# Kernel optimization log

Measured on AMD Instinct MI355X. Metric: run time of the kernel, lower is better.

The kernel has to match this reference:

```python
import jax, jax.numpy as jnp
import numpy as np

N_NODES = 50000
N_EDGES = 625000
D_IN = 128
D_OUT = 128


def setup_inputs() -> dict:
    key = jax.random.key(0)
    k1, k2, k3 = jax.random.split(key, 3)
    x = jax.random.normal(k1, (N_NODES, D_IN), dtype=jnp.float32)
    edge_index = jax.random.randint(k2, (2, N_EDGES), 0, N_NODES, dtype=jnp.int64)
    # torch Linear weight: [d_out, d_in], Kaiming-uniform-ish scale
    weight = jax.random.normal(k3, (D_OUT, D_IN), dtype=jnp.float32) * (1.0 / np.sqrt(D_IN))
    bias = jnp.zeros((D_OUT,), dtype=jnp.float32)
    return {"x": x, "edge_index": edge_index, "weight": weight, "bias": bias}


def reference(x, edge_index, weight, bias):
    N = x.shape[0]
    # gcn_norm: add self-loops with weight 1.0 (improved=False)
    loop = jnp.arange(N, dtype=edge_index.dtype)
    src = jnp.concatenate([edge_index[0], loop])  # [E+N] message sources (x_j)
    dst = jnp.concatenate([edge_index[1], loop])  # [E+N] aggregation targets
    ew = jnp.ones(src.shape[0], dtype=x.dtype)
    # degree computed on target index (col), symmetric normalization
    deg = jax.ops.segment_sum(ew, dst, num_segments=N)
    dinv = jnp.where(deg > 0, jax.lax.rsqrt(deg), 0.0).astype(x.dtype)
    norm = dinv[src] * ew * dinv[dst]  # [E+N]
    # message: norm_e * x[src]; aggregate: scatter-add at dst
    agg = jax.ops.segment_sum(norm[:, None] * x[src], dst, num_segments=N)  # [N, d_in]
    # Linear
    return agg @ weight.T + bias
```

## Files before the change

kernel.cpp:

```cpp
#include <hip/hip_runtime.h>
#include <hip/hip_bf16.h>

#define N_NODES 50000
#define N_EDGES 625000
#define D 128
#define CAP 64
#define NTILES ((N_NODES + 15) / 16)
#define GRID_XW 1024
#define NRANGE 8
#define RSPAN (N_NODES / NRANGE)
#define PART_BLOCKS 1024
#define PART_STRIDE ((PART_BLOCKS / NRANGE) * 256)

typedef __attribute__((ext_vector_type(8))) short bf16x8;
typedef __attribute__((ext_vector_type(4))) float f32x4;

__device__ __forceinline__ float b2f(short s) {
    unsigned u = ((unsigned)(unsigned short)s) << 16;
    return __uint_as_float(u);
}
__device__ __forceinline__ short f2b(float f) {
    union { __hip_bfloat16 h; short s; } cv;
    cv.h = __float2bfloat16(f);
    return cv.s;
}

__global__ void k_zero(int* __restrict__ deg) {
    int i = blockIdx.x * 256 + threadIdx.x;
    if (i < N_NODES) deg[i] = 0;
}

__global__ __launch_bounds__(256) void k_fillpad(const int* __restrict__ src,
                                                 const int* __restrict__ dst,
                                                 int* __restrict__ deg,
                                                 int* __restrict__ colp) {
    int g = blockIdx.x & 7;
    int bg = blockIdx.x >> 3;
    int lo = g * RSPAN, hi = lo + RSPAN;
    for (int e = bg * 256 + threadIdx.x; e < N_EDGES; e += PART_STRIDE) {
        int d = dst[e];
        if (d >= lo && d < hi) {
            int p = atomicAdd(&deg[d], 1);
            if (p < CAP) colp[d * CAP + p] = src[e];
        }
    }
}

__global__ __launch_bounds__(256) void k_xw(const float* __restrict__ x,
                                            const float* __restrict__ w,
                                            const int* __restrict__ deg,
                                            short* __restrict__ y) {
    int t = threadIdx.x;
    int wave = t >> 6, lane = t & 63;
    int c0 = wave * 32;
    int lr = lane & 15;
    int lk = (lane >> 4) * 8;

    bf16x8 wf0[4], wf1[4];
    {
        const float* wp0 = w + (size_t)(c0 + lr) * D + lk;
        const float* wp1 = wp0 + 16 * D;
        #pragma unroll
        for (int ks = 0; ks < 4; ++ks) {
            f32x4 wa0 = *(const f32x4*)(wp0 + ks * 32);
            f32x4 wb0 = *(const f32x4*)(wp0 + ks * 32 + 4);
            f32x4 wa1 = *(const f32x4*)(wp1 + ks * 32);
            f32x4 wb1 = *(const f32x4*)(wp1 + ks * 32 + 4);
            #pragma unroll
            for (int q = 0; q < 4; ++q) {
                wf0[ks][q] = f2b(wa0[q]); wf0[ks][q + 4] = f2b(wb0[q]);
                wf1[ks][q] = f2b(wa1[q]); wf1[ks][q + 4] = f2b(wb1[q]);
            }
        }
    }

    for (int tile = blockIdx.x; tile < NTILES; tile += GRID_XW) {
        int row0 = tile * 16;
        const float* ap = x + (size_t)(row0 + lr) * D + lk;
        f32x4 acc0 = {0.f, 0.f, 0.f, 0.f};
        f32x4 acc1 = {0.f, 0.f, 0.f, 0.f};
        #pragma unroll
        for (int ks = 0; ks < 4; ++ks) {
            f32x4 xa = *(const f32x4*)(ap + ks * 32);
            f32x4 xb = *(const f32x4*)(ap + ks * 32 + 4);
            bf16x8 a;
            #pragma unroll
            for (int q = 0; q < 4; ++q) { a[q] = f2b(xa[q]); a[q + 4] = f2b(xb[q]); }
            acc0 = __builtin_amdgcn_mfma_f32_16x16x32_bf16(a, wf0[ks], acc0, 0, 0, 0);
            acc1 = __builtin_amdgcn_mfma_f32_16x16x32_bf16(a, wf1[ks], acc1, 0, 0, 0);
        }
        int orow = row0 + (lane >> 4) * 4;
        int oc0 = c0 + lr, oc1 = c0 + 16 + lr;
        #pragma unroll
        for (int i = 0; i < 4; ++i) {
            int r = orow + i;
            float ds = rsqrtf((float)(deg[r] + 1));
            y[(size_t)r * D + oc0] = f2b(acc0[i] * ds);
            y[(size_t)r * D + oc1] = f2b(acc1[i] * ds);
        }
    }
}

__global__ __launch_bounds__(256) void k_gather(const short* __restrict__ y,
                                                const int* __restrict__ deg,
                                                const int* __restrict__ colp,
                                                const float* __restrict__ bias,
                                                float* __restrict__ out) {
    int tid = blockIdx.x * 256 + threadIdx.x;
    int n = tid >> 4;
    int sub = threadIdx.x & 15;
    if (n >= N_NODES) return;
    int dn = deg[n];
    float dd = rsqrtf((float)(dn + 1));
    if (dn > CAP) dn = CAP;
    bf16x8 self = *(const bf16x8*)(y + (size_t)n * D + sub * 8);
    float acc0[8], acc1[8];
    #pragma unroll
    for (int q = 0; q < 8; ++q) { acc0[q] = b2f(self[q]); acc1[q] = 0.f; }
    const int* cp = colp + (size_t)n * CAP;
    int j = 0;
    for (; j + 4 <= dn; j += 4) {
        int s0 = cp[j + 0];
        int s1 = cp[j + 1];
        int s2 = cp[j + 2];
        int s3 = cp[j + 3];
        bf16x8 v0 = *(const bf16x8*)(y + (size_t)s0 * D + sub * 8);
        bf16x8 v1 = *(const bf16x8*)(y + (size_t)s1 * D + sub * 8);
        bf16x8 v2 = *(const bf16x8*)(y + (size_t)s2 * D + sub * 8);
        bf16x8 v3 = *(const bf16x8*)(y + (size_t)s3 * D + sub * 8);
        #pragma unroll
        for (int q = 0; q < 8; ++q) {
            acc0[q] += b2f(v0[q]) + b2f(v2[q]);
            acc1[q] += b2f(v1[q]) + b2f(v3[q]);
        }
    }
    for (; j < dn; ++j) {
        int s0 = cp[j];
        bf16x8 v0 = *(const bf16x8*)(y + (size_t)s0 * D + sub * 8);
        #pragma unroll
        for (int q = 0; q < 8; ++q) acc0[q] += b2f(v0[q]);
    }
    const float4* bch = (const float4*)(bias + sub * 8);
    float4 bb0 = bch[0], bb1 = bch[1];
    float4 o0, o1;
    o0.x = dd * (acc0[0] + acc1[0]) + bb0.x; o0.y = dd * (acc0[1] + acc1[1]) + bb0.y;
    o0.z = dd * (acc0[2] + acc1[2]) + bb0.z; o0.w = dd * (acc0[3] + acc1[3]) + bb0.w;
    o1.x = dd * (acc0[4] + acc1[4]) + bb1.x; o1.y = dd * (acc0[5] + acc1[5]) + bb1.y;
    o1.z = dd * (acc0[6] + acc1[6]) + bb1.z; o1.w = dd * (acc0[7] + acc1[7]) + bb1.w;
    float4* op = (float4*)(out + (size_t)n * D + sub * 8);
    op[0] = o0; op[1] = o1;
}

extern "C" void kernel_launch(void* const* d_in, const int* in_sizes, int n_in,
                              void* d_out, int out_size, void* d_ws, size_t ws_size,
                              hipStream_t stream) {
    const float* x    = (const float*)d_in[0];
    const int*   ei   = (const int*)d_in[1];
    const float* w    = (const float*)d_in[2];
    const float* bias = (const float*)d_in[3];
    float* out = (float*)d_out;

    const int* src = ei;
    const int* dst = ei + N_EDGES;

    char* p = (char*)d_ws;
    short* y  = (short*)p;  p += (size_t)N_NODES * D * 2;
    int* deg  = (int*)p;    p += (size_t)N_NODES * 4;
    int* colp = (int*)p;    p += (size_t)N_NODES * CAP * 4;

    k_zero<<<(N_NODES + 255) / 256, 256, 0, stream>>>(deg);
    k_fillpad<<<PART_BLOCKS, 256, 0, stream>>>(src, dst, deg, colp);
    k_xw<<<GRID_XW, 256, 0, stream>>>(x, w, deg, y);
    k_gather<<<((N_NODES * 16) + 255) / 256, 256, 0, stream>>>(y, deg, colp, bias, out);
}
```

Measured before the change: 91.47 us.

## Prefetch next x tile in xw kernel and shuffle-broadcast neighbor indices in gather

In the XW GEMM kernel, the next tile's x rows are loaded into registers before the current tile's MFMAs run, a software-pipelined prefetch meant to hide global load latency. In the gather kernel, each 16-lane group loads up to 16 neighbor indices cooperatively, one per lane, and broadcasts them with __shfl. The unroll is raised to 8 outstanding row loads. This cuts redundant per-lane index loads and adds memory-level parallelism, at the cost of more registers and shuffle instructions.

```diff
diff --git a/kernel.cpp b/kernel.cpp
--- a/kernel.cpp
+++ b/kernel.cpp
@@ -74,22 +74,47 @@
         }
     }
 
-    for (int tile = blockIdx.x; tile < NTILES; tile += GRID_XW) {
-        int row0 = tile * 16;
-        const float* ap = x + (size_t)(row0 + lr) * D + lk;
+    int tile = blockIdx.x;
+    f32x4 xcur0, xcur1, xcur2, xcur3, xcur4, xcur5, xcur6, xcur7;
+    {
+        const float* ap = x + (size_t)(tile * 16 + lr) * D + lk;
+        xcur0 = *(const f32x4*)(ap + 0);   xcur1 = *(const f32x4*)(ap + 4);
+        xcur2 = *(const f32x4*)(ap + 32);  xcur3 = *(const f32x4*)(ap + 36);
+        xcur4 = *(const f32x4*)(ap + 64);  xcur5 = *(const f32x4*)(ap + 68);
+        xcur6 = *(const f32x4*)(ap + 96);  xcur7 = *(const f32x4*)(ap + 100);
+    }
+    for (;;) {
+        int next = tile + GRID_XW;
+        bool has = next < NTILES;
+        f32x4 xn0, xn1, xn2, xn3, xn4, xn5, xn6, xn7;
+        if (has) {
+            const float* ap = x + (size_t)(next * 16 + lr) * D + lk;
+            xn0 = *(const f32x4*)(ap + 0);   xn1 = *(const f32x4*)(ap + 4);
+            xn2 = *(const f32x4*)(ap + 32);  xn3 = *(const f32x4*)(ap + 36);
+            xn4 = *(const f32x4*)(ap + 64);  xn5 = *(const f32x4*)(ap + 68);
+            xn6 = *(const f32x4*)(ap + 96);  xn7 = *(const f32x4*)(ap + 100);
+        }
         f32x4 acc0 = {0.f, 0.f, 0.f, 0.f};
         f32x4 acc1 = {0.f, 0.f, 0.f, 0.f};
-        #pragma unroll
-        for (int ks = 0; ks < 4; ++ks) {
-            f32x4 xa = *(const f32x4*)(ap + ks * 32);
-            f32x4 xb = *(const f32x4*)(ap + ks * 32 + 4);
-            bf16x8 a;
-            #pragma unroll
-            for (int q = 0; q < 4; ++q) { a[q] = f2b(xa[q]); a[q + 4] = f2b(xb[q]); }
-            acc0 = __builtin_amdgcn_mfma_f32_16x16x32_bf16(a, wf0[ks], acc0, 0, 0, 0);
-            acc1 = __builtin_amdgcn_mfma_f32_16x16x32_bf16(a, wf1[ks], acc1, 0, 0, 0);
-        }
-        int orow = row0 + (lane >> 4) * 4;
+        bf16x8 a;
+        #pragma unroll
+        for (int q = 0; q < 4; ++q) { a[q] = f2b(xcur0[q]); a[q + 4] = f2b(xcur1[q]); }
+        acc0 = __builtin_amdgcn_mfma_f32_16x16x32_bf16(a, wf0[0], acc0, 0, 0, 0);
+        acc1 = __builtin_amdgcn_mfma_f32_16x16x32_bf16(a, wf1[0], acc1, 0, 0, 0);
+        #pragma unroll
+        for (int q = 0; q < 4; ++q) { a[q] = f2b(xcur2[q]); a[q + 4] = f2b(xcur3[q]); }
+        acc0 = __builtin_amdgcn_mfma_f32_16x16x32_bf16(a, wf0[1], acc0, 0, 0, 0);
+        acc1 = __builtin_amdgcn_mfma_f32_16x16x32_bf16(a, wf1[1], acc1, 0, 0, 0);
+        #pragma unroll
+        for (int q = 0; q < 4; ++q) { a[q] = f2b(xcur4[q]); a[q + 4] = f2b(xcur5[q]); }
+        acc0 = __builtin_amdgcn_mfma_f32_16x16x32_bf16(a, wf0[2], acc0, 0, 0, 0);
+        acc1 = __builtin_amdgcn_mfma_f32_16x16x32_bf16(a, wf1[2], acc1, 0, 0, 0);
+        #pragma unroll
+        for (int q = 0; q < 4; ++q) { a[q] = f2b(xcur6[q]); a[q + 4] = f2b(xcur7[q]); }
+        acc0 = __builtin_amdgcn_mfma_f32_16x16x32_bf16(a, wf0[3], acc0, 0, 0, 0);
+        acc1 = __builtin_amdgcn_mfma_f32_16x16x32_bf16(a, wf1[3], acc1, 0, 0, 0);
+
+        int orow = tile * 16 + (lane >> 4) * 4;
         int oc0 = c0 + lr, oc1 = c0 + 16 + lr;
         #pragma unroll
         for (int i = 0; i < 4; ++i) {
@@ -98,6 +123,10 @@
             y[(size_t)r * D + oc0] = f2b(acc0[i] * ds);
             y[(size_t)r * D + oc1] = f2b(acc1[i] * ds);
         }
+        if (!has) break;
+        tile = next;
+        xcur0 = xn0; xcur1 = xn1; xcur2 = xn2; xcur3 = xn3;
+        xcur4 = xn4; xcur5 = xn5; xcur6 = xn6; xcur7 = xn7;
     }
 }
 
@@ -109,37 +138,70 @@
     int tid = blockIdx.x * 256 + threadIdx.x;
     int n = tid >> 4;
     int sub = threadIdx.x & 15;
+    int lane = threadIdx.x & 63;
+    int gb = lane & 48;
     if (n >= N_NODES) return;
-    int dn = deg[n];
-    float dd = rsqrtf((float)(dn + 1));
-    if (dn > CAP) dn = CAP;
+    int dn_raw = deg[n];
+    float dd = rsqrtf((float)(dn_raw + 1));
+    int dn = dn_raw < CAP ? dn_raw : CAP;
     bf16x8 self = *(const bf16x8*)(y + (size_t)n * D + sub * 8);
     float acc0[8], acc1[8];
     #pragma unroll
     for (int q = 0; q < 8; ++q) { acc0[q] = b2f(self[q]); acc1[q] = 0.f; }
     const int* cp = colp + (size_t)n * CAP;
-    int j = 0;
-    for (; j + 4 <= dn; j += 4) {
-        int s0 = cp[j + 0];
-        int s1 = cp[j + 1];
-        int s2 = cp[j + 2];
-        int s3 = cp[j + 3];
-        bf16x8 v0 = *(const bf16x8*)(y + (size_t)s0 * D + sub * 8);
-        bf16x8 v1 = *(const bf16x8*)(y + (size_t)s1 * D + sub * 8);
-        bf16x8 v2 = *(const bf16x8*)(y + (size_t)s2 * D + sub * 8);
-        bf16x8 v3 = *(const bf16x8*)(y + (size_t)s3 * D + sub * 8);
-        #pragma unroll
-        for (int q = 0; q < 8; ++q) {
-            acc0[q] += b2f(v0[q]) + b2f(v2[q]);
-            acc1[q] += b2f(v1[q]) + b2f(v3[q]);
-        }
-    }
-    for (; j < dn; ++j) {
-        int s0 = cp[j];
-        bf16x8 v0 = *(const bf16x8*)(y + (size_t)s0 * D + sub * 8);
-        #pragma unroll
-        for (int q = 0; q < 8; ++q) acc0[q] += b2f(v0[q]);
-    }
+
+    for (int bj = 0; bj < dn; bj += 16) {
+        int rem = dn - bj;
+        int m = rem < 16 ? rem : 16;
+        int cidx = (sub < m) ? cp[bj + sub] : 0;
+        int j = 0;
+        for (; j + 8 <= m; j += 8) {
+            int s0 = __shfl(cidx, gb + j + 0);
+            int s1 = __shfl(cidx, gb + j + 1);
+            int s2 = __shfl(cidx, gb + j + 2);
+            int s3 = __shfl(cidx, gb + j + 3);
+            int s4 = __shfl(cidx, gb + j + 4);
+            int s5 = __shfl(cidx, gb + j + 5);
+            int s6 = __shfl(cidx, gb + j + 6);
+            int s7 = __shfl(cidx, gb + j + 7);
+            bf16x8 v0 = *(const bf16x8*)(y + (size_t)s0 * D + sub * 8);
+            bf16x8 v1 = *(const bf16x8*)(y + (size_t)s1 * D + sub * 8);
+            bf16x8 v2 = *(const bf16x8*)(y + (size_t)s2 * D + sub * 8);
+            bf16x8 v3 = *(const bf16x8*)(y + (size_t)s3 * D + sub * 8);
+            bf16x8 v4 = *(const bf16x8*)(y + (size_t)s4 * D + sub * 8);
+            bf16x8 v5 = *(const bf16x8*)(y + (size_t)s5 * D + sub * 8);
+            bf16x8 v6 = *(const bf16x8*)(y + (size_t)s6 * D + sub * 8);
+            bf16x8 v7 = *(const bf16x8*)(y + (size_t)s7 * D + sub * 8);
+            #pragma unroll
+            for (int q = 0; q < 8; ++q) {
+                acc0[q] += b2f(v0[q]) + b2f(v2[q]) + b2f(v4[q]) + b2f(v6[q]);
+                acc1[q] += b2f(v1[q]) + b2f(v3[q]) + b2f(v5[q]) + b2f(v7[q]);
+            }
+        }
+        if (j + 4 <= m) {
+            int s0 = __shfl(cidx, gb + j + 0);
+            int s1 = __shfl(cidx, gb + j + 1);
+            int s2 = __shfl(cidx, gb + j + 2);
+            int s3 = __shfl(cidx, gb + j + 3);
+            bf16x8 v0 = *(const bf16x8*)(y + (size_t)s0 * D + sub * 8);
+            bf16x8 v1 = *(const bf16x8*)(y + (size_t)s1 * D + sub * 8);
+            bf16x8 v2 = *(const bf16x8*)(y + (size_t)s2 * D + sub * 8);
+            bf16x8 v3 = *(const bf16x8*)(y + (size_t)s3 * D + sub * 8);
+            #pragma unroll
+            for (int q = 0; q < 8; ++q) {
+                acc0[q] += b2f(v0[q]) + b2f(v2[q]);
+                acc1[q] += b2f(v1[q]) + b2f(v3[q]);
+            }
+            j += 4;
+        }
+        for (; j < m; ++j) {
+            int s0 = __shfl(cidx, gb + j);
+            bf16x8 v0 = *(const bf16x8*)(y + (size_t)s0 * D + sub * 8);
+            #pragma unroll
+            for (int q = 0; q < 8; ++q) acc0[q] += b2f(v0[q]);
+        }
+    }
+
     const float4* bch = (const float4*)(bias + sub * 8);
     float4 bb0 = bch[0], bb1 = bch[1];
     float4 o0, o1;
```

Measured after the change: 91.74 us. No clear change (+0.3%).

## Fuse fill and XW into one concurrent kernel, move source norm into gather

Applied to the files above, without the earlier changes.

Merges the CSR-pad fill and the X·W GEMM into a single launch whose blocks split by role, so the atomic-heavy fill overlaps the bandwidth-bound GEMM. Because y no longer has the finished degree available, the source-side normalization moves into the gather, which loads neighbor indices cooperatively and broadcasts index and rsqrt(deg) via shuffles. Neighbor indices are stored as 16-bit to halve colp traffic. The cost is extra deg lookups in the gather, and the 16-bit indices only fit because the node count is below 65536.

```diff
diff --git a/kernel.cpp b/kernel.cpp
--- a/kernel.cpp
+++ b/kernel.cpp
@@ -6,11 +6,11 @@
 #define D 128
 #define CAP 64
 #define NTILES ((N_NODES + 15) / 16)
-#define GRID_XW 1024
 #define NRANGE 8
 #define RSPAN (N_NODES / NRANGE)
-#define PART_BLOCKS 1024
-#define PART_STRIDE ((PART_BLOCKS / NRANGE) * 256)
+#define FILL_BLOCKS 1024
+#define XW_BLOCKS 1024
+#define PSTRIDE ((FILL_BLOCKS / NRANGE) * 256)
 
 typedef __attribute__((ext_vector_type(8))) short bf16x8;
 typedef __attribute__((ext_vector_type(4))) float f32x4;
@@ -30,116 +30,134 @@
     if (i < N_NODES) deg[i] = 0;
 }
 
-__global__ __launch_bounds__(256) void k_fillpad(const int* __restrict__ src,
-                                                 const int* __restrict__ dst,
-                                                 int* __restrict__ deg,
-                                                 int* __restrict__ colp) {
-    int g = blockIdx.x & 7;
-    int bg = blockIdx.x >> 3;
-    int lo = g * RSPAN, hi = lo + RSPAN;
-    for (int e = bg * 256 + threadIdx.x; e < N_EDGES; e += PART_STRIDE) {
-        int d = dst[e];
-        if (d >= lo && d < hi) {
-            int p = atomicAdd(&deg[d], 1);
-            if (p < CAP) colp[d * CAP + p] = src[e];
-        }
-    }
-}
-
-__global__ __launch_bounds__(256) void k_xw(const float* __restrict__ x,
-                                            const float* __restrict__ w,
-                                            const int* __restrict__ deg,
-                                            short* __restrict__ y) {
-    int t = threadIdx.x;
-    int wave = t >> 6, lane = t & 63;
-    int c0 = wave * 32;
-    int lr = lane & 15;
-    int lk = (lane >> 4) * 8;
-
-    bf16x8 wf0[4], wf1[4];
-    {
-        const float* wp0 = w + (size_t)(c0 + lr) * D + lk;
-        const float* wp1 = wp0 + 16 * D;
-        #pragma unroll
-        for (int ks = 0; ks < 4; ++ks) {
-            f32x4 wa0 = *(const f32x4*)(wp0 + ks * 32);
-            f32x4 wb0 = *(const f32x4*)(wp0 + ks * 32 + 4);
-            f32x4 wa1 = *(const f32x4*)(wp1 + ks * 32);
-            f32x4 wb1 = *(const f32x4*)(wp1 + ks * 32 + 4);
-            #pragma unroll
-            for (int q = 0; q < 4; ++q) {
-                wf0[ks][q] = f2b(wa0[q]); wf0[ks][q + 4] = f2b(wb0[q]);
-                wf1[ks][q] = f2b(wa1[q]); wf1[ks][q + 4] = f2b(wb1[q]);
+__global__ __launch_bounds__(256) void k_prep(const int* __restrict__ src,
+                                              const int* __restrict__ dst,
+                                              int* __restrict__ deg,
+                                              unsigned short* __restrict__ colp,
+                                              const float* __restrict__ x,
+                                              const float* __restrict__ w,
+                                              short* __restrict__ y) {
+    int b = blockIdx.x;
+    if (b < FILL_BLOCKS) {
+        int g = b & 7;
+        int bg = b >> 3;
+        int lo = g * RSPAN, hi = lo + RSPAN;
+        for (int e = bg * 256 + threadIdx.x; e < N_EDGES; e += PSTRIDE) {
+            int d = dst[e];
+            if (d >= lo && d < hi) {
+                int p = atomicAdd(&deg[d], 1);
+                if (p < CAP) colp[d * CAP + p] = (unsigned short)src[e];
             }
         }
-    }
+    } else {
+        int t = threadIdx.x;
+        int wave = t >> 6, lane = t & 63;
+        int c0 = wave * 32;
+        int lr = lane & 15;
+        int lk = (lane >> 4) * 8;
 
-    for (int tile = blockIdx.x; tile < NTILES; tile += GRID_XW) {
-        int row0 = tile * 16;
-        const float* ap = x + (size_t)(row0 + lr) * D + lk;
-        f32x4 acc0 = {0.f, 0.f, 0.f, 0.f};
-        f32x4 acc1 = {0.f, 0.f, 0.f, 0.f};
-        #pragma unroll
-        for (int ks = 0; ks < 4; ++ks) {
-            f32x4 xa = *(const f32x4*)(ap + ks * 32);
-            f32x4 xb = *(const f32x4*)(ap + ks * 32 + 4);
-            bf16x8 a;
+        bf16x8 wf0[4], wf1[4];
+        {
+            const float* wp0 = w + (size_t)(c0 + lr) * D + lk;
+            const float* wp1 = wp0 + 16 * D;
             #pragma unroll
-            for (int q = 0; q < 4; ++q) { a[q] = f2b(xa[q]); a[q + 4] = f2b(xb[q]); }
-            acc0 = __builtin_amdgcn_mfma_f32_16x16x32_bf16(a, wf0[ks], acc0, 0, 0, 0);
-            acc1 = __builtin_amdgcn_mfma_f32_16x16x32_bf16(a, wf1[ks], acc1, 0, 0, 0);
+            for (int ks = 0; ks < 4; ++ks) {
+                f32x4 wa0 = *(const f32x4*)(wp0 + ks * 32);
+                f32x4 wb0 = *(const f32x4*)(wp0 + ks * 32 + 4);
+                f32x4 wa1 = *(const f32x4*)(wp1 + ks * 32);
+                f32x4 wb1 = *(const f32x4*)(wp1 + ks * 32 + 4);
+                #pragma unroll
+                for (int q = 0; q < 4; ++q) {
+                    wf0[ks][q] = f2b(wa0[q]); wf0[ks][q + 4] = f2b(wb0[q]);
+                    wf1[ks][q] = f2b(wa1[q]); wf1[ks][q + 4] = f2b(wb1[q]);
+                }
+            }
         }
-        int orow = row0 + (lane >> 4) * 4;
-        int oc0 = c0 + lr, oc1 = c0 + 16 + lr;
-        #pragma unroll
-        for (int i = 0; i < 4; ++i) {
-            int r = orow + i;
-            float ds = rsqrtf((float)(deg[r] + 1));
-            y[(size_t)r * D + oc0] = f2b(acc0[i] * ds);
-            y[(size_t)r * D + oc1] = f2b(acc1[i] * ds);
+
+        for (int tile = b - FILL_BLOCKS; tile < NTILES; tile += XW_BLOCKS) {
+            int row0 = tile * 16;
+            const float* ap = x + (size_t)(row0 + lr) * D + lk;
+            f32x4 acc0 = {0.f, 0.f, 0.f, 0.f};
+            f32x4 acc1 = {0.f, 0.f, 0.f, 0.f};
+            #pragma unroll
+            for (int ks = 0; ks < 4; ++ks) {
+                f32x4 xa = *(const f32x4*)(ap + ks * 32);
+                f32x4 xb = *(const f32x4*)(ap + ks * 32 + 4);
+                bf16x8 a;
+                #pragma unroll
+                for (int q = 0; q < 4; ++q) { a[q] = f2b(xa[q]); a[q + 4] = f2b(xb[q]); }
+                acc0 = __builtin_amdgcn_mfma_f32_16x16x32_bf16(a, wf0[ks], acc0, 0, 0, 0);
+                acc1 = __builtin_amdgcn_mfma_f32_16x16x32_bf16(a, wf1[ks], acc1, 0, 0, 0);
+            }
+            int orow = row0 + (lane >> 4) * 4;
+            int oc0 = c0 + lr, oc1 = c0 + 16 + lr;
+            #pragma unroll
+            for (int i = 0; i < 4; ++i) {
+                y[(size_t)(orow + i) * D + oc0] = f2b(acc0[i]);
+                y[(size_t)(orow + i) * D + oc1] = f2b(acc1[i]);
+            }
         }
     }
 }
 
 __global__ __launch_bounds__(256) void k_gather(const short* __restrict__ y,
                                                 const int* __restrict__ deg,
-                                                const int* __restrict__ colp,
+                                                const unsigned short* __restrict__ colp,
                                                 const float* __restrict__ bias,
                                                 float* __restrict__ out) {
     int tid = blockIdx.x * 256 + threadIdx.x;
     int n = tid >> 4;
     int sub = threadIdx.x & 15;
+    int lane = threadIdx.x & 63;
+    int gb = lane & 48;
     if (n >= N_NODES) return;
-    int dn = deg[n];
-    float dd = rsqrtf((float)(dn + 1));
-    if (dn > CAP) dn = CAP;
+    int dn_raw = deg[n];
+    float dd = rsqrtf((float)(dn_raw + 1));
+    int dn = dn_raw < CAP ? dn_raw : CAP;
     bf16x8 self = *(const bf16x8*)(y + (size_t)n * D + sub * 8);
     float acc0[8], acc1[8];
     #pragma unroll
-    for (int q = 0; q < 8; ++q) { acc0[q] = b2f(self[q]); acc1[q] = 0.f; }
-    const int* cp = colp + (size_t)n * CAP;
-    int j = 0;
-    for (; j + 4 <= dn; j += 4) {
-        int s0 = cp[j + 0];
-        int s1 = cp[j + 1];
-        int s2 = cp[j + 2];
-        int s3 = cp[j + 3];
-        bf16x8 v0 = *(const bf16x8*)(y + (size_t)s0 * D + sub * 8);
-        bf16x8 v1 = *(const bf16x8*)(y + (size_t)s1 * D + sub * 8);
-        bf16x8 v2 = *(const bf16x8*)(y + (size_t)s2 * D + sub * 8);
-        bf16x8 v3 = *(const bf16x8*)(y + (size_t)s3 * D + sub * 8);
-        #pragma unroll
-        for (int q = 0; q < 8; ++q) {
-            acc0[q] += b2f(v0[q]) + b2f(v2[q]);
-            acc1[q] += b2f(v1[q]) + b2f(v3[q]);
+    for (int q = 0; q < 8; ++q) { acc0[q] = dd * b2f(self[q]); acc1[q] = 0.f; }
+    const unsigned short* cp = colp + (size_t)n * CAP;
+
+    for (int bj = 0; bj < dn; bj += 16) {
+        int rem = dn - bj;
+        int m = rem < 16 ? rem : 16;
+        int cidx = 0;
+        float cds = 0.f;
+        if (sub < m) {
+            cidx = cp[bj + sub];
+            cds = rsqrtf((float)(deg[cidx] + 1));
+        }
+        int j = 0;
+        for (; j + 4 <= m; j += 4) {
+            int s0 = __shfl(cidx, gb + j + 0);
+            int s1 = __shfl(cidx, gb + j + 1);
+            int s2 = __shfl(cidx, gb + j + 2);
+            int s3 = __shfl(cidx, gb + j + 3);
+            float d0 = __shfl(cds, gb + j + 0);
+            float d1 = __shfl(cds, gb + j + 1);
+            float d2 = __shfl(cds, gb + j + 2);
+            float d3 = __shfl(cds, gb + j + 3);
+            bf16x8 v0 = *(const bf16x8*)(y + (size_t)s0 * D + sub * 8);
+            bf16x8 v1 = *(const bf16x8*)(y + (size_t)s1 * D + sub * 8);
+            bf16x8 v2 = *(const bf16x8*)(y + (size_t)s2 * D + sub * 8);
+            bf16x8 v3 = *(const bf16x8*)(y + (size_t)s3 * D + sub * 8);
+            #pragma unroll
+            for (int q = 0; q < 8; ++q) {
+                acc0[q] += d0 * b2f(v0[q]) + d2 * b2f(v2[q]);
+                acc1[q] += d1 * b2f(v1[q]) + d3 * b2f(v3[q]);
+            }
+        }
+        for (; j < m; ++j) {
+            int s0 = __shfl(cidx, gb + j);
+            float d0 = __shfl(cds, gb + j);
+            bf16x8 v0 = *(const bf16x8*)(y + (size_t)s0 * D + sub * 8);
+            #pragma unroll
+            for (int q = 0; q < 8; ++q) acc0[q] += d0 * b2f(v0[q]);
         }
     }
-    for (; j < dn; ++j) {
-        int s0 = cp[j];
-        bf16x8 v0 = *(const bf16x8*)(y + (size_t)s0 * D + sub * 8);
-        #pragma unroll
-        for (int q = 0; q < 8; ++q) acc0[q] += b2f(v0[q]);
-    }
+
     const float4* bch = (const float4*)(bias + sub * 8);
     float4 bb0 = bch[0], bb1 = bch[1];
     float4 o0, o1;
@@ -164,12 +182,12 @@
     const int* dst = ei + N_EDGES;
 
     char* p = (char*)d_ws;
-    short* y  = (short*)p;  p += (size_t)N_NODES * D * 2;
-    int* deg  = (int*)p;    p += (size_t)N_NODES * 4;
-    int* colp = (int*)p;    p += (size_t)N_NODES * CAP * 4;
+    short* y  = (short*)p;             p += (size_t)N_NODES * D * 2;
+    int* deg  = (int*)p;               p += (size_t)N_NODES * 4;
+    unsigned short* colp = (unsigned short*)p;
+    p += (size_t)N_NODES * CAP * 2;
 
     k_zero<<<(N_NODES + 255) / 256, 256, 0, stream>>>(deg);
-    k_fillpad<<<PART_BLOCKS, 256, 0, stream>>>(src, dst, deg, colp);
-    k_xw<<<GRID_XW, 256, 0, stream>>>(x, w, deg, y);
+    k_prep<<<FILL_BLOCKS + XW_BLOCKS, 256, 0, stream>>>(src, dst, deg, colp, x, w, y);
     k_gather<<<((N_NODES * 16) + 255) / 256, 256, 0, stream>>>(y, deg, colp, bias, out);
 }
```

Result: faster. 77.17 us (-15.6%).
